# Optimization experiments

Hardware: AMD Instinct MI355X
Metric: run time of the kernel (lower is better)

The kernel has to match this reference:

```python
import jax, jax.numpy as jnp
import numpy as np
from jax import lax

B, S, IN, D, E, NH = 8, 128, 512, 1024, 4, 16
DH = D // NH
EPS = 1e-5
SCALE = np.float32(1.0 / np.sqrt(DH))


def setup_inputs() -> dict:
    key = jax.random.key(0)
    ks = iter(jax.random.split(key, 64))
    def rn(shape, scale=0.02):
        return jax.random.normal(next(ks), shape, dtype=jnp.float32) * scale
    z = lambda shape: jnp.zeros(shape, dtype=jnp.float32)
    return {
        "x": jax.random.normal(next(ks), (B, S, IN), dtype=jnp.float32),
        "router_w": rn((IN, E)), "router_b": z((E,)),
        "enc_w1": rn((E, IN, D)), "enc_b1": z((E, D)),
        "enc_w2": rn((E, D, D)), "enc_b2": z((E, D)),
        "enc_g": jnp.ones((E, D), jnp.float32), "enc_beta": z((E, D)),
        "attn_in_w": rn((E, D, 3 * D)), "attn_in_b": z((E, 3 * D)),
        "attn_out_w": rn((E, D, D)), "attn_out_b": z((E, D)),
        "lstm_wi_f": rn((E, D, 4 * D)), "lstm_wh_f": rn((E, D, 4 * D)), "lstm_b_f": z((E, 4 * D)),
        "lstm_wi_b": rn((E, D, 4 * D)), "lstm_wh_b": rn((E, D, 4 * D)), "lstm_b_b": z((E, 4 * D)),
        "sig_w1": rn((E, 2 * D, D)), "sig_b1": z((E, D)),
        "sig_w2": rn((E, D, D)), "sig_b2": z((E, D)),
        "tan_w1": rn((E, 2 * D, D)), "tan_b1": z((E, D)),
        "tan_w2": rn((E, D, D)), "tan_b2": z((E, D)),
        "dec_w1": rn((E, D, D)), "dec_b1": z((E, D)),
        "dec_w2": rn((E, D, IN)), "dec_b2": z((E, IN)),
        "dec_g": jnp.ones((E, IN), jnp.float32), "dec_beta": z((E, IN)),
    }


def _ln(x, g, b):
    m = x.mean(-1, keepdims=True)
    v = ((x - m) ** 2).mean(-1, keepdims=True)
    return (x - m) * lax.rsqrt(v + EPS) * g + b


def _lstm_dir(x, Wi, Wh, b):
    # x: [B,S,D]; single-direction LSTM, returns h sequence [B,S,H]
    bsz = x.shape[0]
    h0 = jnp.zeros((bsz, Wh.shape[0]), x.dtype)
    def step(carry, xt):
        h, c = carry
        zg = xt @ Wi + h @ Wh + b  # [B,4H]; torch gate order i,f,g,o
        i, f, g, o = jnp.split(zg, 4, axis=-1)
        c = jax.nn.sigmoid(f) * c + jax.nn.sigmoid(i) * jnp.tanh(g)
        h = jax.nn.sigmoid(o) * jnp.tanh(c)
        return (h, c), h
    _, hs = lax.scan(step, (h0, h0), jnp.swapaxes(x, 0, 1))
    return jnp.swapaxes(hs, 0, 1)


def _expert(x, p):
    (ew1, eb1, ew2, eb2, eg, ebeta, aiw, aib, aow, aob,
     wif, whf, bf, wibk, whbk, bbk, sw1, sb1, sw2, sb2,
     tw1, tb1, tw2, tb2, dw1, db1, dw2, db2, dg, dbeta) = p
    # encoder MLP + LayerNorm
    h = _ln(jax.nn.relu(x @ ew1 + eb1) @ ew2 + eb2, eg, ebeta)  # [B,S,D]
    # full self-attention (torch MultiheadAttention)
    qkv = h @ aiw + aib
    q, k, v = jnp.split(qkv, 3, axis=-1)
    def heads(t):
        return t.reshape(t.shape[0], t.shape[1], NH, DH).transpose(0, 2, 1, 3)
    q, k, v = heads(q), heads(k), heads(v)
    attn = jax.nn.softmax(jnp.einsum('bhqd,bhkd->bhqk', q, k) * SCALE, axis=-1)
    o = jnp.einsum('bhqk,bhkd->bhqd', attn, v).transpose(0, 2, 1, 3).reshape(h.shape)
    h = o @ aow + aob
    # bidirectional LSTM memory
    hf = _lstm_dir(h, wif, whf, bf)
    hb = _lstm_dir(h[:, ::-1], wibk, whbk, bbk)[:, ::-1]
    mem = jnp.concatenate([hf, hb], axis=-1)  # [B,S,2D]
    # sigmoid/tanh gate branches multiplied
    gate_s = jax.nn.sigmoid(jax.nn.relu(mem @ sw1 + sb1) @ sw2 + sb2)
    gate_t = jnp.tanh(jax.nn.relu(mem @ tw1 + tb1) @ tw2 + tb2)
    g = gate_s * gate_t  # [B,S,D]
    # decoder MLP + LayerNorm back to input_dim
    return _ln(jax.nn.relu(g @ dw1 + db1) @ dw2 + db2, dg, dbeta)


def _forward(x, router_w, router_b, *p):
    outs = jax.vmap(lambda pe: _expert(x, pe))(tuple(p))  # [E,B,S,IN]
    w = jax.nn.softmax(x @ router_w + router_b, axis=-1)  # [B,S,E] token-level routing
    return jnp.einsum('ebsd,bse->bsd', outs, w)


def reference(x, router_w, router_b, enc_w1, enc_b1, enc_w2, enc_b2, enc_g, enc_beta,
              attn_in_w, attn_in_b, attn_out_w, attn_out_b,
              lstm_wi_f, lstm_wh_f, lstm_b_f, lstm_wi_b, lstm_wh_b, lstm_b_b,
              sig_w1, sig_b1, sig_w2, sig_b2, tan_w1, tan_b1, tan_w2, tan_b2,
              dec_w1, dec_b1, dec_w2, dec_b2, dec_g, dec_beta):
    return _forward(x, router_w, router_b, enc_w1, enc_b1, enc_w2, enc_b2, enc_g, enc_beta,
                    attn_in_w, attn_in_b, attn_out_w, attn_out_b,
                    lstm_wi_f, lstm_wh_f, lstm_b_f, lstm_wi_b, lstm_wh_b, lstm_b_b,
                    sig_w1, sig_b1, sig_w2, sig_b2, tan_w1, tan_b1, tan_w2, tan_b2,
                    dec_w1, dec_b1, dec_w2, dec_b2, dec_g, dec_beta)
```

## Files before the change

kernel.cpp:

```cpp
#include <hip/hip_runtime.h>


typedef __attribute__((ext_vector_type(8))) short short8v;
typedef __attribute__((ext_vector_type(4))) float float4v;

__device__ __forceinline__ float bf2f(unsigned short u) {
    unsigned int x = ((unsigned int)u) << 16;
    return __builtin_bit_cast(float, x);
}
__device__ __forceinline__ unsigned short f2bf(float f) {
    unsigned int u = __builtin_bit_cast(unsigned int, f);
    u += 0x7fffu + ((u >> 16) & 1u);
    return (unsigned short)(u >> 16);
}
__device__ __forceinline__ void gload_lds16(const unsigned short* g, unsigned short* lds) {
    __builtin_amdgcn_global_load_lds(
        (const __attribute__((address_space(1))) unsigned int*)g,
        (__attribute__((address_space(3))) unsigned int*)lds, 16, 0, 0);
}

__global__ __launch_bounds__(256) void cvt_bf16_kernel(
    const float* __restrict__ in, unsigned short* __restrict__ out, int n4)
{
    int i = blockIdx.x * 256 + threadIdx.x;
    if (i >= n4) return;
    float4 v = *reinterpret_cast<const float4*>(&in[i * 4]);
    ushort4 o;
    o.x = f2bf(v.x); o.y = f2bf(v.y); o.z = f2bf(v.z); o.w = f2bf(v.w);
    *reinterpret_cast<ushort4*>(&out[i * 4]) = o;
}

__global__ __launch_bounds__(256) void transpose_bf16(
    const float* __restrict__ W, unsigned short* __restrict__ Wt,
    int K, int N, long sWe, long sTe)
{
    __shared__ float tile[32][33];
    int e = blockIdx.z;
    W += (long)e * sWe; Wt += (long)e * sTe;
    int k0 = blockIdx.y * 32, n0 = blockIdx.x * 32;
    int tx = threadIdx.x & 31, ty = threadIdx.x >> 5;
    #pragma unroll
    for (int i = 0; i < 32; i += 8)
        tile[ty + i][tx] = W[(long)(k0 + ty + i) * N + n0 + tx];
    __syncthreads();
    #pragma unroll
    for (int i = 0; i < 32; i += 8)
        Wt[(long)(n0 + ty + i) * K + k0 + tx] = f2bf(tile[tx][ty + i]);
}

__global__ __launch_bounds__(64) void router_kernel(
    const float* __restrict__ x, const float* __restrict__ rw,
    const float* __restrict__ rb, float* __restrict__ router)
{
    int token = blockIdx.x;
    int lane = threadIdx.x;
    float a0 = 0.f, a1 = 0.f, a2 = 0.f, a3 = 0.f;
    const float* xp = x + (long)token * 512;
    for (int i = lane; i < 512; i += 64) {
        float xv = xp[i];
        const float* w = rw + (long)i * 4;
        a0 += xv * w[0]; a1 += xv * w[1]; a2 += xv * w[2]; a3 += xv * w[3];
    }
    #pragma unroll
    for (int off = 32; off; off >>= 1) {
        a0 += __shfl_down(a0, off); a1 += __shfl_down(a1, off);
        a2 += __shfl_down(a2, off); a3 += __shfl_down(a3, off);
    }
    if (lane == 0) {
        a0 += rb[0]; a1 += rb[1]; a2 += rb[2]; a3 += rb[3];
        float m = fmaxf(fmaxf(a0, a1), fmaxf(a2, a3));
        float e0 = __expf(a0 - m), e1 = __expf(a1 - m);
        float e2 = __expf(a2 - m), e3 = __expf(a3 - m);
        float inv = 1.f / (e0 + e1 + e2 + e3);
        *reinterpret_cast<float4*>(&router[token * 4]) =
            make_float4(e0 * inv, e1 * inv, e2 * inv, e3 * inv);
    }
}

template <int OUTBF>
__global__ __launch_bounds__(256) void gemm_bf16(
    const unsigned short* __restrict__ A, const unsigned short* __restrict__ Wt,
    const float* __restrict__ bias, const float* __restrict__ bias2,
    const unsigned short* __restrict__ mul,
    void* __restrict__ Cv, int N, int K, int lda, int nsplit,
    long sAe, long sWe, long sBe, long sMe, long sCe, int act)
{
    __shared__ unsigned short As[128 * 64];
    __shared__ unsigned short Bs[128 * 64];
    int e = blockIdx.z;
    A += (long)e * sAe; Wt += (long)e * sWe;
    bias += (long)e * sBe; bias2 += (long)e * sBe;
    if (mul) mul += (long)e * sMe;
    int tid = threadIdx.x;
    int row0 = blockIdx.y * 128, col0 = blockIdx.x * 128;
    int wid = tid >> 6, lane = tid & 63;
    int wr = wid >> 1, wc = wid & 1;
    int l15 = lane & 15, l4 = lane >> 4;
    int r8 = lane >> 3, sg = lane & 7;
    float4v acc[4][4];
    #pragma unroll
    for (int i = 0; i < 4; ++i)
        #pragma unroll
        for (int j = 0; j < 4; ++j) acc[i][j] = (float4v){0.f, 0.f, 0.f, 0.f};
    for (int k0 = 0; k0 < K; k0 += 64) {
        __syncthreads();
        #pragma unroll
        for (int c = 0; c < 4; ++c) {
            int chunk = wid * 4 + c;
            int rowA = chunk * 8 + r8;
            int segA = (sg ^ (rowA & 7)) * 8;
            gload_lds16(A + (long)(row0 + rowA) * lda + k0 + segA,
                        (unsigned short*)((char*)As + chunk * 1024));
            gload_lds16(Wt + (long)(col0 + rowA) * K + k0 + segA,
                        (unsigned short*)((char*)Bs + chunk * 1024));
        }
        __syncthreads();
        #pragma unroll
        for (int kk = 0; kk < 2; ++kk) {
            short8v af[4], bq[4];
            int bytec = kk * 64 + l4 * 16;
            #pragma unroll
            for (int m = 0; m < 4; ++m) {
                int r = wr * 64 + m * 16 + l15;
                af[m] = *reinterpret_cast<const short8v*>(
                    (char*)As + r * 128 + (bytec ^ ((r & 7) << 4)));
            }
            #pragma unroll
            for (int n = 0; n < 4; ++n) {
                int r = wc * 64 + n * 16 + l15;
                bq[n] = *reinterpret_cast<const short8v*>(
                    (char*)Bs + r * 128 + (bytec ^ ((r & 7) << 4)));
            }
            #pragma unroll
            for (int m = 0; m < 4; ++m)
                #pragma unroll
                for (int n = 0; n < 4; ++n)
                    acc[m][n] = __builtin_amdgcn_mfma_f32_16x16x32_bf16(
                        af[m], bq[n], acc[m][n], 0, 0, 0);
        }
    }
    float* Cf = (float*)Cv + (long)e * sCe;
    unsigned short* Cb = (unsigned short*)Cv + (long)e * sCe;
    #pragma unroll
    for (int n = 0; n < 4; ++n) {
        int col = col0 + wc * 64 + n * 16 + l15;
        float bia = (col < nsplit) ? bias[col] : bias2[col - nsplit];
        #pragma unroll
        for (int m = 0; m < 4; ++m) {
            #pragma unroll
            for (int r = 0; r < 4; ++r) {
                long row = row0 + wr * 64 + m * 16 + l4 * 4 + r;
                float v = acc[m][n][r] + bia;
                if (act == 1) v = fmaxf(v, 0.f);
                else if (act == 2) v = 1.f / (1.f + __expf(-v));
                else if (act == 3) v = tanhf(v);
                if (mul) v *= bf2f(mul[row * N + col]);
                if (OUTBF) Cb[row * N + col] = f2bf(v);
                else       Cf[row * N + col] = v;
            }
        }
    }
}

template <int DIM>
__global__ __launch_bounds__(256) void ln_bf16(
    unsigned short* __restrict__ buf, const float* __restrict__ g,
    const float* __restrict__ beta)
{
    constexpr int PT = DIM / 256;
    __shared__ float sbuf[4];
    int row = blockIdx.x, e = row >> 10;
    unsigned short* p = buf + (long)row * DIM;
    const float* gp = g + (long)e * DIM;
    const float* bp = beta + (long)e * DIM;
    int tid = threadIdx.x;
    float v[PT];
    ushort4 u = *reinterpret_cast<const ushort4*>(p + tid * PT);
    v[0] = bf2f(u.x); v[1] = bf2f(u.y); v[2] = bf2f(u.z); v[3] = bf2f(u.w);
    float s = v[0] + v[1] + v[2] + v[3];
    #pragma unroll
    for (int off = 32; off; off >>= 1) s += __shfl_down(s, off);
    if ((tid & 63) == 0) sbuf[tid >> 6] = s;
    __syncthreads();
    float mean = (sbuf[0] + sbuf[1] + sbuf[2] + sbuf[3]) / (float)DIM;
    __syncthreads();
    float vs = 0.f;
    #pragma unroll
    for (int i = 0; i < PT; ++i) { float d = v[i] - mean; vs += d * d; }
    #pragma unroll
    for (int off = 32; off; off >>= 1) vs += __shfl_down(vs, off);
    if ((tid & 63) == 0) sbuf[tid >> 6] = vs;
    __syncthreads();
    float var = (sbuf[0] + sbuf[1] + sbuf[2] + sbuf[3]) / (float)DIM;
    float rstd = rsqrtf(var + 1e-5f);
    ushort4 o;
    o.x = f2bf((v[0] - mean) * rstd * gp[tid * PT + 0] + bp[tid * PT + 0]);
    o.y = f2bf((v[1] - mean) * rstd * gp[tid * PT + 1] + bp[tid * PT + 1]);
    o.z = f2bf((v[2] - mean) * rstd * gp[tid * PT + 2] + bp[tid * PT + 2]);
    o.w = f2bf((v[3] - mean) * rstd * gp[tid * PT + 3] + bp[tid * PT + 3]);
    *reinterpret_cast<ushort4*>(p + tid * PT) = o;
}

template <int DIM>
__global__ __launch_bounds__(256) void ln_kernel(
    float* __restrict__ buf, const float* __restrict__ g,
    const float* __restrict__ beta)
{
    constexpr int PT = DIM / 256;
    __shared__ float sbuf[4];
    int row = blockIdx.x, e = row >> 10;
    float* p = buf + (long)row * DIM;
    const float* gp = g + (long)e * DIM;
    const float* bp = beta + (long)e * DIM;
    int tid = threadIdx.x;
    float v[PT];
    float s = 0.f;
    #pragma unroll
    for (int i = 0; i < PT; ++i) { v[i] = p[tid + i * 256]; s += v[i]; }
    #pragma unroll
    for (int off = 32; off; off >>= 1) s += __shfl_down(s, off);
    if ((tid & 63) == 0) sbuf[tid >> 6] = s;
    __syncthreads();
    float mean = (sbuf[0] + sbuf[1] + sbuf[2] + sbuf[3]) / (float)DIM;
    __syncthreads();
    float vs = 0.f;
    #pragma unroll
    for (int i = 0; i < PT; ++i) { float d = v[i] - mean; vs += d * d; }
    #pragma unroll
    for (int off = 32; off; off >>= 1) vs += __shfl_down(vs, off);
    if ((tid & 63) == 0) sbuf[tid >> 6] = vs;
    __syncthreads();
    float var = (sbuf[0] + sbuf[1] + sbuf[2] + sbuf[3]) / (float)DIM;
    float rstd = rsqrtf(var + 1e-5f);
    #pragma unroll
    for (int i = 0; i < PT; ++i)
        p[tid + i * 256] = (v[i] - mean) * rstd * gp[tid + i * 256] + bp[tid + i * 256];
}

__global__ __launch_bounds__(128) void attn_bf16(
    const unsigned short* __restrict__ qkv, unsigned short* __restrict__ o)
{
    __shared__ __align__(16) float Ks[128][64];
    __shared__ __align__(16) float Vs[128][64];
    int id = blockIdx.x;
    int hd = id & 15, b = (id >> 4) & 7, e = id >> 7;
    int tid = threadIdx.x;
    const long base = ((long)e * 1024 + b * 128) * 3072 + hd * 64;
    #pragma unroll
    for (int i = 0; i < 8; ++i) {
        int idx = i * 128 + tid;
        int row = idx >> 3, f8 = (idx & 7) * 8;
        short8v kv = *reinterpret_cast<const short8v*>(&qkv[base + (long)row * 3072 + 1024 + f8]);
        short8v vv = *reinterpret_cast<const short8v*>(&qkv[base + (long)row * 3072 + 2048 + f8]);
        #pragma unroll
        for (int j = 0; j < 8; ++j) {
            Ks[row][f8 + j] = bf2f((unsigned short)kv[j]);
            Vs[row][f8 + j] = bf2f((unsigned short)vv[j]);
        }
    }
    __syncthreads();
    float q[64];
    #pragma unroll
    for (int f = 0; f < 8; ++f) {
        short8v qv = *reinterpret_cast<const short8v*>(&qkv[base + (long)tid * 3072 + f * 8]);
        #pragma unroll
        for (int j = 0; j < 8; ++j) q[f * 8 + j] = bf2f((unsigned short)qv[j]);
    }
    float m = -__builtin_huge_valf(), l = 0.f;
    float oa[64];
    #pragma unroll
    for (int d = 0; d < 64; ++d) oa[d] = 0.f;
    for (int j = 0; j < 128; ++j) {
        float s = 0.f;
        #pragma unroll
        for (int d = 0; d < 64; ++d) s = fmaf(q[d], Ks[j][d], s);
        s *= 0.125f;
        float mn = fmaxf(m, s);
        float corr = __expf(m - mn);
        float pj = __expf(s - mn);
        l = l * corr + pj;
        #pragma unroll
        for (int d = 0; d < 64; ++d) oa[d] = oa[d] * corr + pj * Vs[j][d];
        m = mn;
    }
    float inv = 1.f / l;
    unsigned short* op = o + ((long)e * 1024 + b * 128 + tid) * 1024 + hd * 64;
    #pragma unroll
    for (int f = 0; f < 8; ++f) {
        short8v ov;
        #pragma unroll
        for (int j = 0; j < 8; ++j) ov[j] = (short)f2bf(oa[f * 8 + j] * inv);
        *reinterpret_cast<short8v*>(&op[f * 8]) = ov;
    }
}

__global__ __launch_bounds__(512, 4) void lstm_persistent(
    const unsigned short* __restrict__ pre, const unsigned short* __restrict__ whtf,
    const unsigned short* __restrict__ whtb, unsigned short* __restrict__ hstate,
    unsigned short* __restrict__ memb, unsigned int* __restrict__ sync)
{
    __shared__ unsigned short hA[16 * 1024];
    __shared__ float zred[4][2][8][16];
    int bid = blockIdx.x;
    int ed = bid & 7, cb = bid >> 3;
    int e = ed >> 1, dir = ed & 1;
    const unsigned short* Wt = (dir ? whtb : whtf) + (long)e * 4096 * 1024;
    const unsigned short* pre_ed = pre + (long)ed * 1024 * 4096;
    unsigned int* arr = sync + ed * 64;
    unsigned int* go  = sync + 512 + ed * 64;
    int tid = threadIdx.x;
    int w = tid >> 6, lane = tid & 63, l15 = lane & 15, l4 = lane >> 4;
    int g = w >> 1, kh = w & 1;
    short8v wf[16];
    const unsigned short* wp =
        Wt + ((long)(g * 1024 + cb * 16 + l15)) * 1024 + kh * 512 + l4 * 8;
    #pragma unroll
    for (int ks = 0; ks < 16; ++ks)
        wf[ks] = *reinterpret_cast<const short8v*>(wp + ks * 32);
    short8v z8 = {0, 0, 0, 0, 0, 0, 0, 0};
    for (int i = tid; i < 8 * 128; i += 512) {
        int r = 8 + (i >> 7), sb = (i & 127) * 16;
        *reinterpret_cast<short8v*>((char*)hA + r * 2048 + (sb ^ ((r & 7) << 4))) = z8;
    }
    float c0 = 0.f, c1 = 0.f;
    int gp = tid & 7, gb = tid >> 3;
    for (int s = 0; s < 128; ++s) {
        int t = dir ? 127 - s : s;
        const unsigned long long* hin64 = reinterpret_cast<const unsigned long long*>(
            hstate + (long)(s & 1) * 65536 + (long)ed * 8192);
        __syncthreads();
        #pragma unroll
        for (int i = 0; i < 4; ++i) {
            int idx = tid + 512 * i;
            unsigned long long v = __hip_atomic_load(
                hin64 + idx, __ATOMIC_RELAXED, __HIP_MEMORY_SCOPE_AGENT);
            int r = idx >> 8, sb = (idx & 255) * 8;
            *reinterpret_cast<unsigned long long*>(
                (char*)hA + r * 2048 + (sb ^ ((r & 7) << 4))) = v;
        }
        float pz[8];
        if (tid < 64) {
            const unsigned short* prow =
                pre_ed + ((long)gb * 128 + t) * 4096 + cb * 16 + gp * 2;
            #pragma unroll
            for (int gg = 0; gg < 4; ++gg) {
                unsigned int u = *reinterpret_cast<const unsigned int*>(prow + gg * 1024);
                pz[gg * 2]     = bf2f((unsigned short)(u & 0xffff));
                pz[gg * 2 + 1] = bf2f((unsigned short)(u >> 16));
            }
        }
        __syncthreads();
        float4v acc = (float4v){0.f, 0.f, 0.f, 0.f};
        int abase = l15 * 2048, aswz = (l15 & 7) << 4;
        #pragma unroll
        for (int ks = 0; ks < 16; ++ks) {
            short8v a = *reinterpret_cast<const short8v*>(
                (char*)hA + abase + (((kh * 512 + ks * 32) * 2 + l4 * 16) ^ aswz));
            acc = __builtin_amdgcn_mfma_f32_16x16x32_bf16(a, wf[ks], acc, 0, 0, 0);
        }
        if (l4 < 2) {
            #pragma unroll
            for (int r = 0; r < 4; ++r)
                zred[g][kh][l4 * 4 + r][l15] = acc[r];
        }
        __syncthreads();
        if (tid < 64) {
            int col0 = gp * 2;
            float h2[2];
            #pragma unroll
            for (int cc = 0; cc < 2; ++cc) {
                int col = col0 + cc;
                float zi = zred[0][0][gb][col] + zred[0][1][gb][col] + pz[0 + cc];
                float zf = zred[1][0][gb][col] + zred[1][1][gb][col] + pz[2 + cc];
                float zg = zred[2][0][gb][col] + zred[2][1][gb][col] + pz[4 + cc];
                float zo = zred[3][0][gb][col] + zred[3][1][gb][col] + pz[6 + cc];
                float ig = 1.f / (1.f + __expf(-zi));
                float fg = 1.f / (1.f + __expf(-zf));
                float gv = tanhf(zg);
                float og = 1.f / (1.f + __expf(-zo));
                float cv = cc ? c1 : c0;
                cv = fg * cv + ig * gv;
                if (cc) c1 = cv; else c0 = cv;
                h2[cc] = og * tanhf(cv);
            }
            unsigned int hv = (unsigned int)f2bf(h2[0]) | ((unsigned int)f2bf(h2[1]) << 16);
            int hcol = cb * 16 + col0;
            unsigned int* hout32 = reinterpret_cast<unsigned int*>(
                hstate + (long)((s & 1) ^ 1) * 65536 + (long)ed * 8192);
            __hip_atomic_store(hout32 + (gb * 1024 + hcol) / 2, hv,
                               __ATOMIC_RELAXED, __HIP_MEMORY_SCOPE_AGENT);
            *reinterpret_cast<unsigned int*>(
                memb + (((long)e * 8 + gb) * 128 + t) * 2048 + dir * 1024 + hcol) = hv;
        }
        __syncthreads();
        if (cb == 0) {
            if (tid > 0 && tid < 64) {
                while (__hip_atomic_load(arr + tid, __ATOMIC_RELAXED,
                                         __HIP_MEMORY_SCOPE_AGENT) < (unsigned)(s + 1))
                    __builtin_amdgcn_s_sleep(1);
            }
            if (tid < 64) {
                asm volatile("s_waitcnt vmcnt(0)" ::: "memory");
                if (tid == 0)
                    __hip_atomic_store(go, (unsigned)(s + 1), __ATOMIC_RELAXED,
                                       __HIP_MEMORY_SCOPE_AGENT);
            }
        } else if (tid == 0) {
            __hip_atomic_store(arr + cb, (unsigned)(s + 1), __ATOMIC_RELAXED,
                               __HIP_MEMORY_SCOPE_AGENT);
            while (__hip_atomic_load(go, __ATOMIC_RELAXED,
                                     __HIP_MEMORY_SCOPE_AGENT) < (unsigned)(s + 1))
                __builtin_amdgcn_s_sleep(2);
        }
    }
}

__global__ __launch_bounds__(256) void combine_kernel(
    const float* __restrict__ outs, const float* __restrict__ router,
    float* __restrict__ out)
{
    int idx = blockIdx.x * 256 + threadIdx.x;
    int token = idx >> 7, q = (idx & 127) * 4;
    float4 r = *reinterpret_cast<const float4*>(&router[token * 4]);
    const float* bp = outs + (long)token * 512 + q;
    float4 v0 = *reinterpret_cast<const float4*>(bp);
    float4 v1 = *reinterpret_cast<const float4*>(bp + 524288);
    float4 v2 = *reinterpret_cast<const float4*>(bp + 1048576);
    float4 v3 = *reinterpret_cast<const float4*>(bp + 1572864);
    float4 a;
    a.x = r.x * v0.x + r.y * v1.x + r.z * v2.x + r.w * v3.x;
    a.y = r.x * v0.y + r.y * v1.y + r.z * v2.y + r.w * v3.y;
    a.z = r.x * v0.z + r.y * v1.z + r.z * v2.z + r.w * v3.z;
    a.w = r.x * v0.w + r.y * v1.w + r.z * v2.w + r.w * v3.w;
    *reinterpret_cast<float4*>(&out[(long)token * 512 + q]) = a;
}

extern "C" void kernel_launch(void* const* d_in, const int* in_sizes, int n_in,
                              void* d_out, int out_size, void* d_ws, size_t ws_size,
                              hipStream_t stream)
{
    (void)in_sizes; (void)n_in; (void)out_size; (void)ws_size;
    const float* x        = (const float*)d_in[0];
    const float* router_w = (const float*)d_in[1];
    const float* router_b = (const float*)d_in[2];
    const float* enc_w1   = (const float*)d_in[3];
    const float* enc_b1   = (const float*)d_in[4];
    const float* enc_w2   = (const float*)d_in[5];
    const float* enc_b2   = (const float*)d_in[6];
    const float* enc_g    = (const float*)d_in[7];
    const float* enc_beta = (const float*)d_in[8];
    const float* aiw      = (const float*)d_in[9];
    const float* aib      = (const float*)d_in[10];
    const float* aow      = (const float*)d_in[11];
    const float* aob      = (const float*)d_in[12];
    const float* wif      = (const float*)d_in[13];
    const float* whf      = (const float*)d_in[14];
    const float* bfv      = (const float*)d_in[15];
    const float* wib      = (const float*)d_in[16];
    const float* whb      = (const float*)d_in[17];
    const float* bbv      = (const float*)d_in[18];
    const float* sw1      = (const float*)d_in[19];
    const float* sb1      = (const float*)d_in[20];
    const float* sw2      = (const float*)d_in[21];
    const float* sb2      = (const float*)d_in[22];
    const float* tw1      = (const float*)d_in[23];
    const float* tb1      = (const float*)d_in[24];
    const float* tw2      = (const float*)d_in[25];
    const float* tb2      = (const float*)d_in[26];
    const float* dw1      = (const float*)d_in[27];
    const float* db1      = (const float*)d_in[28];
    const float* dw2      = (const float*)d_in[29];
    const float* db2      = (const float*)d_in[30];
    const float* dg       = (const float*)d_in[31];
    const float* dbeta    = (const float*)d_in[32];
    float* out = (float*)d_out;

    const long m = 1024L * 1024L;
    unsigned short* U = (unsigned short*)d_ws;
    unsigned short* ew1T = U;
    unsigned short* ew2T = U + 2 * m;
    unsigned short* aiwT = U + 6 * m;
    unsigned short* aowT = U + 18 * m;
    unsigned short* wifT = U + 22 * m;
    unsigned short* wibT = U + 38 * m;
    unsigned short* whtf = U + 54 * m;
    unsigned short* whtb = U + 70 * m;
    unsigned short* gw1T = U + 86 * m;
    unsigned short* sw2T = U + 102 * m;
    unsigned short* tw2T = U + 106 * m;
    unsigned short* dw1T = U + 110 * m;
    unsigned short* dw2T = U + 114 * m;
    unsigned short* xb   = U + 116 * m;
    unsigned short* hbuf = xb + 524288;
    unsigned short* t1   = hbuf + 4 * m;
    unsigned short* t2   = t1 + 4 * m;
    unsigned short* pre  = t2 + 4 * m;
    unsigned short* memb = pre + 32 * m;
    unsigned short* hstate = memb + 8 * m;
    float* F      = (float*)(U + 170 * m);
    float* outs   = F;
    float* router = outs + 2 * m;
    unsigned int* syncv = (unsigned int*)(router + 4096);

    hipMemsetAsync(hstate, 0, 65536 * sizeof(unsigned short), stream);
    hipMemsetAsync(syncv, 0, 1024 * sizeof(unsigned int), stream);

    cvt_bf16_kernel<<<512, 256, 0, stream>>>(x, xb, 131072);
    transpose_bf16<<<dim3(32, 16, 4), 256, 0, stream>>>(enc_w1, ew1T, 512, 1024, 512 * 1024L, 512 * 1024L);
    transpose_bf16<<<dim3(32, 32, 4), 256, 0, stream>>>(enc_w2, ew2T, 1024, 1024, m, m);
    transpose_bf16<<<dim3(96, 32, 4), 256, 0, stream>>>(aiw, aiwT, 1024, 3072, 3 * m, 3 * m);
    transpose_bf16<<<dim3(32, 32, 4), 256, 0, stream>>>(aow, aowT, 1024, 1024, m, m);
    transpose_bf16<<<dim3(128, 32, 4), 256, 0, stream>>>(wif, wifT, 1024, 4096, 4 * m, 4 * m);
    transpose_bf16<<<dim3(128, 32, 4), 256, 0, stream>>>(wib, wibT, 1024, 4096, 4 * m, 4 * m);
    transpose_bf16<<<dim3(128, 32, 4), 256, 0, stream>>>(whf, whtf, 1024, 4096, 4 * m, 4 * m);
    transpose_bf16<<<dim3(128, 32, 4), 256, 0, stream>>>(whb, whtb, 1024, 4096, 4 * m, 4 * m);
    transpose_bf16<<<dim3(32, 64, 4), 256, 0, stream>>>(sw1, gw1T, 2048, 1024, 2 * m, 4 * m);
    transpose_bf16<<<dim3(32, 64, 4), 256, 0, stream>>>(tw1, gw1T + 2 * m, 2048, 1024, 2 * m, 4 * m);
    transpose_bf16<<<dim3(32, 32, 4), 256, 0, stream>>>(sw2, sw2T, 1024, 1024, m, m);
    transpose_bf16<<<dim3(32, 32, 4), 256, 0, stream>>>(tw2, tw2T, 1024, 1024, m, m);
    transpose_bf16<<<dim3(32, 32, 4), 256, 0, stream>>>(dw1, dw1T, 1024, 1024, m, m);
    transpose_bf16<<<dim3(16, 32, 4), 256, 0, stream>>>(dw2, dw2T, 1024, 512, 512 * 1024L, 512 * 1024L);

    router_kernel<<<1024, 64, 0, stream>>>(x, router_w, router_b, router);

    gemm_bf16<1><<<dim3(8, 8, 4), 256, 0, stream>>>(xb, ew1T, enc_b1, enc_b1, nullptr, t1,
        1024, 512, 512, 1024, 0L, 512 * 1024L, 1024L, 0L, m, 1);
    gemm_bf16<1><<<dim3(8, 8, 4), 256, 0, stream>>>(t1, ew2T, enc_b2, enc_b2, nullptr, hbuf,
        1024, 1024, 1024, 1024, m, m, 1024L, 0L, m, 0);
    ln_bf16<1024><<<4096, 256, 0, stream>>>(hbuf, enc_g, enc_beta);
    gemm_bf16<1><<<dim3(24, 8, 4), 256, 0, stream>>>(hbuf, aiwT, aib, aib, nullptr, pre,
        3072, 1024, 1024, 3072, m, 3 * m, 3072L, 0L, 3 * m, 0);
    attn_bf16<<<512, 128, 0, stream>>>(pre, t1);
    gemm_bf16<1><<<dim3(8, 8, 4), 256, 0, stream>>>(t1, aowT, aob, aob, nullptr, hbuf,
        1024, 1024, 1024, 1024, m, m, 1024L, 0L, m, 0);
    gemm_bf16<1><<<dim3(32, 8, 4), 256, 0, stream>>>(hbuf, wifT, bfv, bfv, nullptr, pre,
        4096, 1024, 1024, 4096, m, 4 * m, 4096L, 0L, 8 * m, 0);
    gemm_bf16<1><<<dim3(32, 8, 4), 256, 0, stream>>>(hbuf, wibT, bbv, bbv, nullptr, pre + 4 * m,
        4096, 1024, 1024, 4096, m, 4 * m, 4096L, 0L, 8 * m, 0);
    lstm_persistent<<<512, 512, 0, stream>>>(pre, whtf, whtb, hstate, memb, syncv);
    unsigned short* g1o = pre;
    gemm_bf16<1><<<dim3(16, 8, 4), 256, 0, stream>>>(memb, gw1T, sb1, tb1, nullptr, g1o,
        2048, 2048, 2048, 1024, 2 * m, 4 * m, 1024L, 0L, 2 * m, 1);
    gemm_bf16<1><<<dim3(8, 8, 4), 256, 0, stream>>>(g1o, sw2T, sb2, sb2, nullptr, t2,
        1024, 1024, 2048, 1024, 2 * m, m, 1024L, 0L, m, 2);
    gemm_bf16<1><<<dim3(8, 8, 4), 256, 0, stream>>>(g1o + 1024, tw2T, tb2, tb2, t2, hbuf,
        1024, 1024, 2048, 1024, 2 * m, m, 1024L, m, m, 3);
    gemm_bf16<1><<<dim3(8, 8, 4), 256, 0, stream>>>(hbuf, dw1T, db1, db1, nullptr, t1,
        1024, 1024, 1024, 1024, m, m, 1024L, 0L, m, 1);
    gemm_bf16<0><<<dim3(4, 8, 4), 256, 0, stream>>>(t1, dw2T, db2, db2, nullptr, outs,
        512, 1024, 1024, 512, m, 512 * 1024L, 512L, 0L, 512 * 1024L, 0);
    ln_kernel<512><<<4096, 256, 0, stream>>>(outs, dg, dbeta);
    combine_kernel<<<512, 256, 0, stream>>>(outs, router, out);
}
```

Before: 1.375 ms.

## Batch transposes, double-buffer GEMM LDS, merge LSTM input GEMMs, flatten LSTM barrier

The fourteen weight-transpose launches become one job-table kernel. The bf16 GEMM gets double-buffered LDS so the next K-tile loads while MFMAs run. The forward and backward LSTM input projections are merged into one GEMM over the concatenated weights, and the LSTM kernel now reads the interleaved layout. The LSTM step sync changes from a leader-based two-phase barrier to every block polling all arrival counters. Together these cut launch overhead and memory latency stalls, at the cost of doubled GEMM LDS use (lower occupancy) and more atomic polling traffic.

```diff
diff --git a/kernel.cpp b/kernel.cpp
--- a/kernel.cpp
+++ b/kernel.cpp
@@ -30,14 +30,29 @@
     *reinterpret_cast<ushort4*>(&out[i * 4]) = o;
 }
 
-__global__ __launch_bounds__(256) void transpose_bf16(
-    const float* __restrict__ W, unsigned short* __restrict__ Wt,
-    int K, int N, long sWe, long sTe)
+struct TransJobs {
+    const float* src[14];
+    unsigned short* dst[14];
+    int K[14], N[14];
+    int prefix[15];
+    long sWe[14], sTe[14];
+};
+
+__global__ __launch_bounds__(256) void transpose_all(TransJobs J)
 {
     __shared__ float tile[32][33];
-    int e = blockIdx.z;
-    W += (long)e * sWe; Wt += (long)e * sTe;
-    int k0 = blockIdx.y * 32, n0 = blockIdx.x * 32;
+    int bid = blockIdx.x;
+    int j = 0;
+    #pragma unroll
+    for (int i = 0; i < 14; ++i) if (bid >= J.prefix[i + 1]) j = i + 1;
+    int lb = bid - J.prefix[j];
+    int K = J.K[j], N = J.N[j];
+    int tn = N >> 5, tk = K >> 5;
+    int e = lb / (tn * tk), rem = lb % (tn * tk);
+    int ky = rem / tn, nx = rem % tn;
+    const float* W = J.src[j] + (long)e * J.sWe[j];
+    unsigned short* Wt = J.dst[j] + (long)e * J.sTe[j];
+    int k0 = ky * 32, n0 = nx * 32;
     int tx = threadIdx.x & 31, ty = threadIdx.x >> 5;
     #pragma unroll
     for (int i = 0; i < 32; i += 8)
@@ -85,8 +100,8 @@
     void* __restrict__ Cv, int N, int K, int lda, int nsplit,
     long sAe, long sWe, long sBe, long sMe, long sCe, int act)
 {
-    __shared__ unsigned short As[128 * 64];
-    __shared__ unsigned short Bs[128 * 64];
+    __shared__ unsigned short As[2][128 * 64];
+    __shared__ unsigned short Bs[2][128 * 64];
     int e = blockIdx.z;
     A += (long)e * sAe; Wt += (long)e * sWe;
     bias += (long)e * sBe; bias2 += (long)e * sBe;
@@ -102,19 +117,31 @@
     for (int i = 0; i < 4; ++i)
         #pragma unroll
         for (int j = 0; j < 4; ++j) acc[i][j] = (float4v){0.f, 0.f, 0.f, 0.f};
-    for (int k0 = 0; k0 < K; k0 += 64) {
-        __syncthreads();
+
+    auto STAGE = [&](int buf, int k0) {
         #pragma unroll
         for (int c = 0; c < 4; ++c) {
             int chunk = wid * 4 + c;
             int rowA = chunk * 8 + r8;
             int segA = (sg ^ (rowA & 7)) * 8;
             gload_lds16(A + (long)(row0 + rowA) * lda + k0 + segA,
-                        (unsigned short*)((char*)As + chunk * 1024));
+                        (unsigned short*)((char*)As[buf] + chunk * 1024));
             gload_lds16(Wt + (long)(col0 + rowA) * K + k0 + segA,
-                        (unsigned short*)((char*)Bs + chunk * 1024));
-        }
-        __syncthreads();
+                        (unsigned short*)((char*)Bs[buf] + chunk * 1024));
+        }
+    };
+    int nt = K >> 6;
+    STAGE(0, 0);
+    for (int t = 0; t < nt; ++t) {
+        int cur = t & 1;
+        if (t + 1 < nt) {
+            STAGE(cur ^ 1, (t + 1) << 6);
+            asm volatile("s_waitcnt vmcnt(8)" ::: "memory");
+        } else {
+            asm volatile("s_waitcnt vmcnt(0)" ::: "memory");
+        }
+        __builtin_amdgcn_s_barrier();
+        __builtin_amdgcn_sched_barrier(0);
         #pragma unroll
         for (int kk = 0; kk < 2; ++kk) {
             short8v af[4], bq[4];
@@ -123,13 +150,13 @@
             for (int m = 0; m < 4; ++m) {
                 int r = wr * 64 + m * 16 + l15;
                 af[m] = *reinterpret_cast<const short8v*>(
-                    (char*)As + r * 128 + (bytec ^ ((r & 7) << 4)));
+                    (char*)As[cur] + r * 128 + (bytec ^ ((r & 7) << 4)));
             }
             #pragma unroll
             for (int n = 0; n < 4; ++n) {
                 int r = wc * 64 + n * 16 + l15;
                 bq[n] = *reinterpret_cast<const short8v*>(
-                    (char*)Bs + r * 128 + (bytec ^ ((r & 7) << 4)));
+                    (char*)Bs[cur] + r * 128 + (bytec ^ ((r & 7) << 4)));
             }
             #pragma unroll
             for (int m = 0; m < 4; ++m)
@@ -138,6 +165,8 @@
                     acc[m][n] = __builtin_amdgcn_mfma_f32_16x16x32_bf16(
                         af[m], bq[n], acc[m][n], 0, 0, 0);
         }
+        __builtin_amdgcn_sched_barrier(0);
+        __builtin_amdgcn_s_barrier();
     }
     float* Cf = (float*)Cv + (long)e * sCe;
     unsigned short* Cb = (unsigned short*)Cv + (long)e * sCe;
@@ -305,9 +334,7 @@
     int ed = bid & 7, cb = bid >> 3;
     int e = ed >> 1, dir = ed & 1;
     const unsigned short* Wt = (dir ? whtb : whtf) + (long)e * 4096 * 1024;
-    const unsigned short* pre_ed = pre + (long)ed * 1024 * 4096;
     unsigned int* arr = sync + ed * 64;
-    unsigned int* go  = sync + 512 + ed * 64;
     int tid = threadIdx.x;
     int w = tid >> 6, lane = tid & 63, l15 = lane & 15, l4 = lane >> 4;
     int g = w >> 1, kh = w & 1;
@@ -341,7 +368,7 @@
         float pz[8];
         if (tid < 64) {
             const unsigned short* prow =
-                pre_ed + ((long)gb * 128 + t) * 4096 + cb * 16 + gp * 2;
+                pre + (((long)e * 1024) + gb * 128 + t) * 8192 + dir * 4096 + cb * 16 + gp * 2;
             #pragma unroll
             for (int gg = 0; gg < 4; ++gg) {
                 unsigned int u = *reinterpret_cast<const unsigned int*>(prow + gg * 1024);
@@ -392,25 +419,15 @@
             *reinterpret_cast<unsigned int*>(
                 memb + (((long)e * 8 + gb) * 128 + t) * 2048 + dir * 1024 + hcol) = hv;
         }
+        if (s == 127) break;
         __syncthreads();
-        if (cb == 0) {
-            if (tid > 0 && tid < 64) {
-                while (__hip_atomic_load(arr + tid, __ATOMIC_RELAXED,
-                                         __HIP_MEMORY_SCOPE_AGENT) < (unsigned)(s + 1))
-                    __builtin_amdgcn_s_sleep(1);
-            }
-            if (tid < 64) {
-                asm volatile("s_waitcnt vmcnt(0)" ::: "memory");
-                if (tid == 0)
-                    __hip_atomic_store(go, (unsigned)(s + 1), __ATOMIC_RELAXED,
-                                       __HIP_MEMORY_SCOPE_AGENT);
-            }
-        } else if (tid == 0) {
+        if (tid == 0)
             __hip_atomic_store(arr + cb, (unsigned)(s + 1), __ATOMIC_RELAXED,
                                __HIP_MEMORY_SCOPE_AGENT);
-            while (__hip_atomic_load(go, __ATOMIC_RELAXED,
+        if (tid < 64) {
+            while (__hip_atomic_load(arr + tid, __ATOMIC_RELAXED,
                                      __HIP_MEMORY_SCOPE_AGENT) < (unsigned)(s + 1))
-                __builtin_amdgcn_s_sleep(2);
+                __builtin_amdgcn_s_sleep(1);
         }
     }
 }
@@ -481,8 +498,7 @@
     unsigned short* ew2T = U + 2 * m;
     unsigned short* aiwT = U + 6 * m;
     unsigned short* aowT = U + 18 * m;
-    unsigned short* wifT = U + 22 * m;
-    unsigned short* wibT = U + 38 * m;
+    unsigned short* wiT  = U + 22 * m;
     unsigned short* whtf = U + 54 * m;
     unsigned short* whtb = U + 70 * m;
     unsigned short* gw1T = U + 86 * m;
@@ -506,20 +522,31 @@
     hipMemsetAsync(syncv, 0, 1024 * sizeof(unsigned int), stream);
 
     cvt_bf16_kernel<<<512, 256, 0, stream>>>(x, xb, 131072);
-    transpose_bf16<<<dim3(32, 16, 4), 256, 0, stream>>>(enc_w1, ew1T, 512, 1024, 512 * 1024L, 512 * 1024L);
-    transpose_bf16<<<dim3(32, 32, 4), 256, 0, stream>>>(enc_w2, ew2T, 1024, 1024, m, m);
-    transpose_bf16<<<dim3(96, 32, 4), 256, 0, stream>>>(aiw, aiwT, 1024, 3072, 3 * m, 3 * m);
-    transpose_bf16<<<dim3(32, 32, 4), 256, 0, stream>>>(aow, aowT, 1024, 1024, m, m);
-    transpose_bf16<<<dim3(128, 32, 4), 256, 0, stream>>>(wif, wifT, 1024, 4096, 4 * m, 4 * m);
-    transpose_bf16<<<dim3(128, 32, 4), 256, 0, stream>>>(wib, wibT, 1024, 4096, 4 * m, 4 * m);
-    transpose_bf16<<<dim3(128, 32, 4), 256, 0, stream>>>(whf, whtf, 1024, 4096, 4 * m, 4 * m);
-    transpose_bf16<<<dim3(128, 32, 4), 256, 0, stream>>>(whb, whtb, 1024, 4096, 4 * m, 4 * m);
-    transpose_bf16<<<dim3(32, 64, 4), 256, 0, stream>>>(sw1, gw1T, 2048, 1024, 2 * m, 4 * m);
-    transpose_bf16<<<dim3(32, 64, 4), 256, 0, stream>>>(tw1, gw1T + 2 * m, 2048, 1024, 2 * m, 4 * m);
-    transpose_bf16<<<dim3(32, 32, 4), 256, 0, stream>>>(sw2, sw2T, 1024, 1024, m, m);
-    transpose_bf16<<<dim3(32, 32, 4), 256, 0, stream>>>(tw2, tw2T, 1024, 1024, m, m);
-    transpose_bf16<<<dim3(32, 32, 4), 256, 0, stream>>>(dw1, dw1T, 1024, 1024, m, m);
-    transpose_bf16<<<dim3(16, 32, 4), 256, 0, stream>>>(dw2, dw2T, 1024, 512, 512 * 1024L, 512 * 1024L);
+    {
+        TransJobs J;
+        const float* srcs[14] = {enc_w1, enc_w2, aiw, aow, wif, wib, whf, whb,
+                                 sw1, tw1, sw2, tw2, dw1, dw2};
+        unsigned short* dsts[14] = {ew1T, ew2T, aiwT, aowT, wiT, wiT + 4096 * 1024L,
+                                    whtf, whtb, gw1T, gw1T + 2 * m, sw2T, tw2T, dw1T, dw2T};
+        int Ks[14] = {512, 1024, 1024, 1024, 1024, 1024, 1024, 1024,
+                      2048, 2048, 1024, 1024, 1024, 1024};
+        int Ns[14] = {1024, 1024, 3072, 1024, 4096, 4096, 4096, 4096,
+                      1024, 1024, 1024, 1024, 1024, 512};
+        long sWes[14] = {512 * 1024L, m, 3 * m, m, 4 * m, 4 * m, 4 * m, 4 * m,
+                         2 * m, 2 * m, m, m, m, 512 * 1024L};
+        long sTes[14] = {512 * 1024L, m, 3 * m, m, 8 * m, 8 * m, 4 * m, 4 * m,
+                         4 * m, 4 * m, m, m, m, 512 * 1024L};
+        int pfx = 0;
+        J.prefix[0] = 0;
+        for (int i = 0; i < 14; ++i) {
+            J.src[i] = srcs[i]; J.dst[i] = dsts[i];
+            J.K[i] = Ks[i]; J.N[i] = Ns[i];
+            J.sWe[i] = sWes[i]; J.sTe[i] = sTes[i];
+            pfx += (Ns[i] >> 5) * (Ks[i] >> 5) * 4;
+            J.prefix[i + 1] = pfx;
+        }
+        transpose_all<<<pfx, 256, 0, stream>>>(J);
+    }
 
     router_kernel<<<1024, 64, 0, stream>>>(x, router_w, router_b, router);
 
@@ -533,10 +560,8 @@
     attn_bf16<<<512, 128, 0, stream>>>(pre, t1);
     gemm_bf16<1><<<dim3(8, 8, 4), 256, 0, stream>>>(t1, aowT, aob, aob, nullptr, hbuf,
         1024, 1024, 1024, 1024, m, m, 1024L, 0L, m, 0);
-    gemm_bf16<1><<<dim3(32, 8, 4), 256, 0, stream>>>(hbuf, wifT, bfv, bfv, nullptr, pre,
-        4096, 1024, 1024, 4096, m, 4 * m, 4096L, 0L, 8 * m, 0);
-    gemm_bf16<1><<<dim3(32, 8, 4), 256, 0, stream>>>(hbuf, wibT, bbv, bbv, nullptr, pre + 4 * m,
-        4096, 1024, 1024, 4096, m, 4 * m, 4096L, 0L, 8 * m, 0);
+    gemm_bf16<1><<<dim3(64, 8, 4), 256, 0, stream>>>(hbuf, wiT, bfv, bbv, nullptr, pre,
+        8192, 1024, 1024, 4096, m, 8 * m, 4096L, 0L, 8 * m, 0);
     lstm_persistent<<<512, 512, 0, stream>>>(pre, whtf, whtb, hstate, memb, syncv);
     unsigned short* g1o = pre;
     gemm_bf16<1><<<dim3(16, 8, 4), 256, 0, stream>>>(memb, gw1T, sb1, tb1, nullptr, g1o,
```

Result: faster. 1.306 ms (-5.0%).
